# Kernel tuning notes

Measured on AMD Instinct MI355X. Metric: run time of the kernel, lower is better.

## Reference

```python
import jax, jax.numpy as jnp
import numpy as np

N = 100000      # nodes
E = 1000000     # edges
IN = 512
H = [512, 256]
C = 64          # n_classes
K = 10          # propagation steps
ALPHA = 0.1


def _glorot(key, shape):
    lim = np.sqrt(6.0 / (shape[0] + shape[1])).astype(np.float32)
    return jax.random.uniform(key, shape, jnp.float32, -lim, lim)


def setup_inputs() -> dict:
    key = jax.random.key(0)
    ks = jax.random.split(key, 6)
    features = jax.random.normal(ks[0], (N, IN), jnp.float32)
    edge_index = jax.random.randint(ks[1], (2, E), 0, N)  # int32/64 src,dst
    W0 = _glorot(ks[2], (H[0], IN)); b0 = jnp.zeros((H[0],), jnp.float32)
    W1 = _glorot(ks[3], (H[1], H[0])); b1 = jnp.zeros((H[1],), jnp.float32)
    W2 = _glorot(ks[4], (C, H[1])); b2 = jnp.zeros((C,), jnp.float32)
    return dict(features=features, edge_index=edge_index,
                W0=W0, b0=b0, W1=W1, b1=b1, W2=W2, b2=b2)


def _appnp(h, src, dst):
    # DGL APPNPConv: symmetric normalization D_out^{-1/2} A D_in^{-1/2},
    # degrees clamped to min 1; h_{t+1} = (1-a) * norm_agg + a * h_0.
    ones = jnp.ones(src.shape, h.dtype)
    deg_out = jax.ops.segment_sum(ones, src, num_segments=N)
    deg_in = jax.ops.segment_sum(ones, dst, num_segments=N)
    norm_src = jnp.maximum(deg_out, 1.0) ** -0.5  # [N]
    norm_dst = jnp.maximum(deg_in, 1.0) ** -0.5   # [N]
    h0 = h
    for _ in range(K):
        msg = (h * norm_src[:, None])[src]                     # [E, C] gather
        agg = jax.ops.segment_sum(msg, dst, num_segments=N)    # [N, C] scatter-add
        h = (1.0 - ALPHA) * agg * norm_dst[:, None] + ALPHA * h0
    return h


def reference(features, edge_index, W0, b0, W1, b1, W2, b2):
    src, dst = edge_index[0], edge_index[1]
    h = jax.nn.relu(features @ W0.T + b0)   # [N, 512]
    h = jax.nn.relu(h @ W1.T + b1)          # [N, 256]
    h = h @ W2.T + b2                       # [N, 64] logits
    return _appnp(h, src, dst)
```

## Files before the change

kernel.cpp:

```cpp
#include <hip/hip_runtime.h>
#include <hip/hip_bf16.h>

#define NN_NODES 100000
#define NE_EDGES 1000000
#define D_IN 512
#define D_H0 512
#define D_H1 256
#define D_C  64

using f32x4  = __attribute__((ext_vector_type(4))) float;
using h16x8  = __attribute__((ext_vector_type(8))) _Float16;

static __device__ __forceinline__ void gll16(const _Float16* g, _Float16* l){
    __builtin_amdgcn_global_load_lds(
        (const __attribute__((address_space(1))) unsigned int*)g,
        (__attribute__((address_space(3))) unsigned int*)l, 16, 0, 0);
}

__global__ __launch_bounds__(256) void tof16_tiled_kernel(
    const float* __restrict__ w, _Float16* __restrict__ o, int R, int K)
{
    int i = blockIdx.x * 256 + threadIdx.x;
    int n8 = R * (K >> 3);
    if (i >= n8) return;
    int kd = K >> 3;
    int r  = i / kd;
    int c0 = (i - r * kd) * 8;
    const f32x4 a = *(const f32x4*)(w + (size_t)r * K + c0);
    const f32x4 b = *(const f32x4*)(w + (size_t)r * K + c0 + 4);
    h16x8 h;
    #pragma unroll
    for (int j = 0; j < 4; j++){
        h[j]   = (_Float16)a[j];
        h[j+4] = (_Float16)b[j];
    }
    size_t off = ((size_t)(r >> 7) * (K >> 5) + (c0 >> 5)) * 4096
               + (size_t)(r & 127) * 32 + (c0 & 31);
    *(h16x8*)(o + off) = h;
}

template<bool RELU, int OMODE, int BN_T, int NBN, int KK>
__global__ __launch_bounds__(256, 4) void gemm_kernel(
    const _Float16* __restrict__ A,
    const _Float16* __restrict__ B,
    const float* __restrict__ bias,
    void* __restrict__ O1, _Float16* __restrict__ O2, const float* __restrict__ scale,
    int M, int NNc, int xq, int xr)
{
    constexpr int NTK  = KK / 32;
    constexpr int NF   = BN_T / 32;
    constexpr int BBLK = BN_T / 16;
    constexpr int TOT  = 8 + BBLK;
    constexpr int LPW  = TOT / 4;

    __shared__ _Float16 sA[2][128 * 32];
    __shared__ _Float16 sB[2][BN_T * 32];

    const int tid  = threadIdx.x;
    const int lane = tid & 63;
    const int wv   = tid >> 6;
    const int wm   = wv >> 1;
    const int wn   = wv & 1;
    const int fr   = lane & 15;
    const int fc   = lane >> 4;

    const int bid = blockIdx.x;
    const int xcd = bid & 7;
    const int i8  = bid >> 3;
    const int L   = ((xcd < xr) ? xcd * (xq + 1) : xr * (xq + 1) + (xcd - xr) * xq) + i8;
    const int mt  = L / NBN;
    const int bn  = L - mt * NBN;
    const int bm0 = mt * 128;
    const int bn0 = bn * BN_T;

    const int bslab = bn0 >> 7;
    const int binsl = bn0 & 127;

    const int loff = (lane >> 2) * 32 + ((lane & 3) ^ ((lane >> 3) & 3)) * 8;

    f32x4 acc[4][NF] = {};

    auto stage = [&](int b, int t){
        const _Float16* as = A + ((size_t)mt * NTK + t) * 4096;
        const _Float16* bs = B + ((size_t)bslab * NTK + t) * 4096 + binsl * 32;
        #pragma unroll
        for (int u = 0; u < LPW; u++){
            int idx = u * 4 + wv;
            if (idx < 8) gll16(as + idx * 512 + loff, sA[b] + idx * 512);
            else         gll16(bs + (idx - 8) * 512 + loff, sB[b] + (idx - 8) * 512);
        }
    };

    auto compute = [&](int b){
        h16x8 bf[NF];
        #pragma unroll
        for (int nf = 0; nf < NF; nf++){
            int r = wn * (BN_T / 2) + nf * 16 + fr;
            int c = (fc ^ ((r >> 1) & 3)) * 8;
            bf[nf] = *(const h16x8*)&sB[b][r * 32 + c];
        }
        h16x8 af[4];
        #pragma unroll
        for (int mf = 0; mf < 4; mf++){
            int r = wm * 64 + mf * 16 + fr;
            int c = (fc ^ ((r >> 1) & 3)) * 8;
            af[mf] = *(const h16x8*)&sA[b][r * 32 + c];
        }
        __builtin_amdgcn_s_setprio(1);
        #pragma unroll
        for (int mf = 0; mf < 4; mf++)
            #pragma unroll
            for (int nf = 0; nf < NF; nf++)
                acc[mf][nf] = __builtin_amdgcn_mfma_f32_16x16x32_f16(af[mf], bf[nf], acc[mf][nf], 0, 0, 0);
        __builtin_amdgcn_s_setprio(0);
    };

    stage(0, 0);
    __syncthreads();
    int cur = 0;
    for (int t = 0; t < NTK; t++){
        if (t + 1 < NTK) stage(cur ^ 1, t + 1);
        compute(cur);
        __syncthreads();
        cur ^= 1;
    }

    #pragma unroll
    for (int mf = 0; mf < 4; mf++){
        #pragma unroll
        for (int nf = 0; nf < NF; nf++){
            #pragma unroll
            for (int r = 0; r < 4; r++){
                int rg = bm0 + wm * 64 + mf * 16 + fc * 4 + r;
                int cg = bn0 + wn * (BN_T / 2) + nf * 16 + fr;
                if (rg < M){
                    float v = acc[mf][nf][r] + bias[cg];
                    if constexpr (RELU) v = fmaxf(v, 0.f);
                    if constexpr (OMODE == 1){
                        size_t o = ((size_t)mt * (NNc >> 5) + (cg >> 5)) * 4096
                                 + (size_t)(rg & 127) * 32 + (cg & 31);
                        ((_Float16*)O1)[o] = (_Float16)v;
                    } else {
                        ((_Float16*)O1)[(size_t)rg * NNc + cg] = (_Float16)v;
                        O2[(size_t)rg * NNc + cg] = (_Float16)(v * scale[rg]);
                    }
                }
            }
        }
    }
}

__global__ __launch_bounds__(512, 2) void gemm23_kernel(
    const _Float16* __restrict__ A,
    const _Float16* __restrict__ B1,
    const _Float16* __restrict__ B2,
    const float* __restrict__ bias1,
    const float* __restrict__ bias2,
    _Float16* __restrict__ h0h, _Float16* __restrict__ h0s,
    const float* __restrict__ nsrc,
    int M, int xq, int xr)
{
    constexpr int NTK = 16;
    __shared__ _Float16 smem[49152];

    const int tid  = threadIdx.x;
    const int lane = tid & 63;
    const int wv   = tid >> 6;
    const int wm   = wv >> 2;
    const int wn   = wv & 3;
    const int fr   = lane & 15;
    const int fc   = lane >> 4;

    const int bid = blockIdx.x;
    const int xcd = bid & 7;
    const int i8  = bid >> 3;
    const int mt  = ((xcd < xr) ? xcd * (xq + 1) : xr * (xq + 1) + (xcd - xr) * xq) + i8;
    const int bm0 = mt * 128;

    const int loff = (lane >> 2) * 32 + ((lane & 3) ^ ((lane >> 3) & 3)) * 8;

    _Float16* sW2 = smem + 32768;

    #pragma unroll
    for (int u = 0; u < 4; u++){
        int idx = u * 8 + wv;
        int k = idx >> 2, rb = idx & 3;
        gll16(B2 + (size_t)k * 4096 + rb * 512 + loff, sW2 + k * 2048 + rb * 512);
    }

    auto sA = [&](int b){ return smem + b * 12288; };
    auto sB = [&](int b){ return smem + b * 12288 + 4096; };

    auto stage = [&](int b, int t){
        #pragma unroll
        for (int u = 0; u < 3; u++){
            int idx = u * 8 + wv;
            if (idx < 8){
                gll16(A + ((size_t)mt * NTK + t) * 4096 + idx * 512 + loff,
                      sA(b) + idx * 512);
            } else {
                int rb = idx - 8;
                gll16(B1 + ((size_t)(rb >> 3) * NTK + t) * 4096 + (rb & 7) * 512 + loff,
                      sB(b) + rb * 512);
            }
        }
    };

    f32x4 acc[4][4] = {};

    auto compute = [&](int b){
        h16x8 bf[4];
        #pragma unroll
        for (int nf = 0; nf < 4; nf++){
            int r = wn * 64 + nf * 16 + fr;
            int c = (fc ^ ((r >> 1) & 3)) * 8;
            bf[nf] = *(const h16x8*)&sB(b)[r * 32 + c];
        }
        h16x8 af[4];
        #pragma unroll
        for (int mf = 0; mf < 4; mf++){
            int r = wm * 64 + mf * 16 + fr;
            int c = (fc ^ ((r >> 1) & 3)) * 8;
            af[mf] = *(const h16x8*)&sA(b)[r * 32 + c];
        }
        __builtin_amdgcn_s_setprio(1);
        #pragma unroll
        for (int mf = 0; mf < 4; mf++)
            #pragma unroll
            for (int nf = 0; nf < 4; nf++)
                acc[mf][nf] = __builtin_amdgcn_mfma_f32_16x16x32_f16(af[mf], bf[nf], acc[mf][nf], 0, 0, 0);
        __builtin_amdgcn_s_setprio(0);
    };

    stage(0, 0);
    __syncthreads();
    int cur = 0;
    for (int t = 0; t < NTK; t++){
        if (t + 1 < NTK) stage(cur ^ 1, t + 1);
        compute(cur);
        __syncthreads();
        cur ^= 1;
    }

    #pragma unroll
    for (int mf = 0; mf < 4; mf++){
        #pragma unroll
        for (int nf = 0; nf < 4; nf++){
            #pragma unroll
            for (int r = 0; r < 4; r++){
                int row = wm * 64 + mf * 16 + fc * 4 + r;
                int col = wn * 64 + nf * 16 + fr;
                float v = fmaxf(acc[mf][nf][r] + bias1[col], 0.f);
                int ci = col & 31;
                int sw = ((ci >> 3) ^ ((row >> 1) & 3)) * 8 + (ci & 7);
                smem[(col >> 5) * 4096 + row * 32 + sw] = (_Float16)v;
            }
        }
    }
    __syncthreads();

    f32x4 acc2[4] = {};
    #pragma unroll
    for (int kk = 0; kk < 8; kk++){
        int ar = wv * 16 + fr;
        int ac = (fc ^ ((ar >> 1) & 3)) * 8;
        h16x8 af = *(const h16x8*)&smem[kk * 4096 + ar * 32 + ac];
        #pragma unroll
        for (int nf = 0; nf < 4; nf++){
            int br = nf * 16 + fr;
            int bc = (fc ^ ((br >> 1) & 3)) * 8;
            h16x8 bf = *(const h16x8*)&sW2[kk * 2048 + br * 32 + bc];
            acc2[nf] = __builtin_amdgcn_mfma_f32_16x16x32_f16(af, bf, acc2[nf], 0, 0, 0);
        }
    }
    #pragma unroll
    for (int nf = 0; nf < 4; nf++){
        #pragma unroll
        for (int r = 0; r < 4; r++){
            int rg = bm0 + wv * 16 + fc * 4 + r;
            int cg = nf * 16 + fr;
            if (rg < M){
                float v = acc2[nf][r] + bias2[cg];
                h0h[(size_t)rg * D_C + cg] = (_Float16)v;
                h0s[(size_t)rg * D_C + cg] = (_Float16)(v * nsrc[rg]);
            }
        }
    }
}

__global__ void degrees_kernel(const int* __restrict__ src, const int* __restrict__ dst,
                               int* __restrict__ dout, int* __restrict__ din){
    int e = blockIdx.x * blockDim.x + threadIdx.x;
    if (e < NE_EDGES){
        atomicAdd(&dout[src[e]], 1);
        atomicAdd(&din[dst[e]], 1);
    }
}

__global__ void norm_kernel(const int* __restrict__ dout, const int* __restrict__ din,
                            float* __restrict__ ns, float* __restrict__ nd, int n){
    int i = blockIdx.x * blockDim.x + threadIdx.x;
    if (i < n){
        ns[i] = rsqrtf((float)(dout[i] > 1 ? dout[i] : 1));
        nd[i] = rsqrtf((float)(din[i]  > 1 ? din[i]  : 1));
    }
}

__global__ __launch_bounds__(256) void scan1_kernel(const int* __restrict__ din,
                                                    int* __restrict__ part,
                                                    int* __restrict__ bsum, int n){
    __shared__ int s[256];
    int i = blockIdx.x * 256 + threadIdx.x;
    int v = (i < n) ? din[i] : 0;
    s[threadIdx.x] = v;
    __syncthreads();
    for (int off = 1; off < 256; off <<= 1){
        int t = (threadIdx.x >= off) ? s[threadIdx.x - off] : 0;
        __syncthreads();
        s[threadIdx.x] += t;
        __syncthreads();
    }
    if (i < n) part[i] = s[threadIdx.x];
    if (threadIdx.x == 255) bsum[blockIdx.x] = s[255];
}

__global__ __launch_bounds__(512) void scan2_kernel(int* __restrict__ bsum, int nb){
    __shared__ int s[512];
    int v = (threadIdx.x < nb) ? bsum[threadIdx.x] : 0;
    s[threadIdx.x] = v;
    __syncthreads();
    for (int off = 1; off < 512; off <<= 1){
        int t = (threadIdx.x >= off) ? s[threadIdx.x - off] : 0;
        __syncthreads();
        s[threadIdx.x] += t;
        __syncthreads();
    }
    if (threadIdx.x < nb) bsum[threadIdx.x] = s[threadIdx.x];
}

__global__ void scan3_kernel(const int* __restrict__ part, const int* __restrict__ din,
                             const int* __restrict__ bsum, int* __restrict__ offs,
                             int* __restrict__ cur, int n){
    int i = blockIdx.x * 256 + threadIdx.x;
    if (i < n){
        int base = (blockIdx.x > 0) ? bsum[blockIdx.x - 1] : 0;
        int excl = base + part[i] - din[i];
        offs[i] = excl;
        cur[i]  = excl;
    }
}

__global__ void fill_kernel(const int* __restrict__ src, const int* __restrict__ dst,
                            int* __restrict__ cur, int* __restrict__ csr){
    int e = blockIdx.x * blockDim.x + threadIdx.x;
    if (e < NE_EDGES){
        int d = dst[e];
        int pos = atomicAdd(&cur[d], 1);
        csr[pos] = src[e];
    }
}

__global__ __launch_bounds__(256) void propagate_kernel(
    const _Float16* __restrict__ hs, const _Float16* __restrict__ h0h,
    float* __restrict__ hout, _Float16* __restrict__ houts,
    const int* __restrict__ offs, const int* __restrict__ din,
    const int* __restrict__ csr,
    const float* __restrict__ ns, const float* __restrict__ nd)
{
    int t    = blockIdx.x * 256 + threadIdx.x;
    int node = t >> 3;
    int gl   = t & 7;
    if (node >= NN_NODES) return;
    int start = offs[node];
    int deg   = din[node];
    float ndv = 0.9f * nd[node];
    float nsv = ns[node];
    h16x8 h0v = *(const h16x8*)(h0h + (size_t)node * D_C + gl * 8);
    float acc[8] = {};
    int j = 0;
    for (; j + 4 <= deg; j += 4){
        int s0 = csr[start + j];
        int s1 = csr[start + j + 1];
        int s2 = csr[start + j + 2];
        int s3 = csr[start + j + 3];
        h16x8 v0 = *(const h16x8*)(hs + (size_t)s0 * D_C + gl * 8);
        h16x8 v1 = *(const h16x8*)(hs + (size_t)s1 * D_C + gl * 8);
        h16x8 v2 = *(const h16x8*)(hs + (size_t)s2 * D_C + gl * 8);
        h16x8 v3 = *(const h16x8*)(hs + (size_t)s3 * D_C + gl * 8);
        #pragma unroll
        for (int i = 0; i < 8; i++)
            acc[i] += ((float)v0[i] + (float)v1[i]) + ((float)v2[i] + (float)v3[i]);
    }
    for (; j < deg; j++){
        int s0 = csr[start + j];
        h16x8 v0 = *(const h16x8*)(hs + (size_t)s0 * D_C + gl * 8);
        #pragma unroll
        for (int i = 0; i < 8; i++) acc[i] += (float)v0[i];
    }
    float out[8];
    #pragma unroll
    for (int i = 0; i < 8; i++) out[i] = acc[i] * ndv + 0.1f * (float)h0v[i];
    if (houts){
        h16x8 o;
        #pragma unroll
        for (int i = 0; i < 8; i++) o[i] = (_Float16)(out[i] * nsv);
        *(h16x8*)(houts + (size_t)node * D_C + gl * 8) = o;
    }
    if (hout){
        f32x4 oa, ob;
        #pragma unroll
        for (int i = 0; i < 4; i++){ oa[i] = out[i]; ob[i] = out[i + 4]; }
        *(f32x4*)(hout + (size_t)node * D_C + gl * 8)     = oa;
        *(f32x4*)(hout + (size_t)node * D_C + gl * 8 + 4) = ob;
    }
}

extern "C" void kernel_launch(void* const* d_in, const int* in_sizes, int n_in,
                              void* d_out, int out_size, void* d_ws, size_t ws_size,
                              hipStream_t stream)
{
    const float* features = (const float*)d_in[0];
    const int*   edge     = (const int*)d_in[1];
    const float* W0 = (const float*)d_in[2];
    const float* b0 = (const float*)d_in[3];
    const float* W1 = (const float*)d_in[4];
    const float* b1 = (const float*)d_in[5];
    const float* W2 = (const float*)d_in[6];
    const float* b2 = (const float*)d_in[7];
    const int* src = edge;
    const int* dst = edge + NE_EDGES;

    char* p = (char*)d_ws;
    auto alloc = [&](size_t bytes) -> char* {
        char* r = p;
        p += (bytes + 255) & ~(size_t)255;
        return r;
    };

    const int MT = (NN_NODES + 127) / 128;
    const size_t FEAT_T = (size_t)MT * 16 * 4096 * 2;
    const size_t HBUFH  = (size_t)NN_NODES * D_C * 2;

    _Float16* w0f = (_Float16*)alloc((size_t)4 * 16 * 4096 * 2);
    _Float16* w1f = (_Float16*)alloc((size_t)2 * 16 * 4096 * 2);
    _Float16* w2f = (_Float16*)alloc((size_t)1 * 8  * 4096 * 2);
    char* R1 = alloc(FEAT_T);
    char* R2 = alloc(FEAT_T);
    int*   deg_out = (int*)alloc((size_t)NN_NODES * 4);
    int*   deg_in  = (int*)alloc((size_t)NN_NODES * 4);
    float* nsrc    = (float*)alloc((size_t)NN_NODES * 4);
    float* ndst    = (float*)alloc((size_t)NN_NODES * 4);
    int*   part    = (int*)alloc((size_t)NN_NODES * 4);
    int*   bsum    = (int*)alloc(2048);
    int*   offs    = (int*)alloc((size_t)NN_NODES * 4);
    int*   cur     = (int*)alloc((size_t)NN_NODES * 4);
    int*   csr     = (int*)alloc((size_t)NE_EDGES * 4);
    if ((size_t)(p - (char*)d_ws) > ws_size) return;

    _Float16* fhf  = (_Float16*)R1;
    _Float16* act1 = (_Float16*)R2;
    _Float16* h0h  = (_Float16*)R1;
    _Float16* h0s  = (_Float16*)(R1 + HBUFH);
    _Float16* hAs  = (_Float16*)(R1 + 2 * HBUFH);
    _Float16* hBs  = (_Float16*)(R1 + 3 * HBUFH);

    hipMemsetAsync(deg_out, 0, (size_t)NN_NODES * 4, stream);
    hipMemsetAsync(deg_in,  0, (size_t)NN_NODES * 4, stream);
    degrees_kernel<<<(NE_EDGES + 255) / 256, 256, 0, stream>>>(src, dst, deg_out, deg_in);
    norm_kernel<<<(NN_NODES + 255) / 256, 256, 0, stream>>>(deg_out, deg_in, nsrc, ndst, NN_NODES);
    int nb = (NN_NODES + 255) / 256;
    scan1_kernel<<<nb, 256, 0, stream>>>(deg_in, part, bsum, NN_NODES);
    scan2_kernel<<<1, 512, 0, stream>>>(bsum, nb);
    scan3_kernel<<<nb, 256, 0, stream>>>(part, deg_in, bsum, offs, cur, NN_NODES);
    fill_kernel<<<(NE_EDGES + 255) / 256, 256, 0, stream>>>(src, dst, cur, csr);

    tof16_tiled_kernel<<<(NN_NODES * D_IN / 8 + 255) / 256, 256, 0, stream>>>(
        features, fhf, NN_NODES, D_IN);
    tof16_tiled_kernel<<<(D_H0 * D_IN / 8 + 255) / 256, 256, 0, stream>>>(W0, w0f, D_H0, D_IN);
    tof16_tiled_kernel<<<(D_H1 * D_H0 / 8 + 255) / 256, 256, 0, stream>>>(W1, w1f, D_H1, D_H0);
    tof16_tiled_kernel<<<(D_C * D_H1 / 8 + 255) / 256, 256, 0, stream>>>(W2, w2f, D_C, D_H1);

    {
        int nwg = MT * 8;
        gemm_kernel<true, 1, 64, 8, 512><<<nwg, 256, 0, stream>>>(
            fhf, w0f, b0, act1, nullptr, nullptr, NN_NODES, D_H0, nwg / 8, nwg % 8);
    }
    {
        int nwg = MT;
        gemm23_kernel<<<nwg, 512, 0, stream>>>(
            act1, w1f, w2f, b1, b2, h0h, h0s, nsrc, NN_NODES, nwg / 8, nwg % 8);
    }

    const _Float16* curs = h0s;
    _Float16* bufss[2] = { hAs, hBs };
    int pb = (NN_NODES * 8 + 255) / 256;
    for (int it = 0; it < 10; it++){
        float*    out  = (it == 9) ? (float*)d_out : nullptr;
        _Float16* outs = (it == 9) ? nullptr       : bufss[it & 1];
        propagate_kernel<<<pb, 256, 0, stream>>>(curs, h0h, out, outs, offs, deg_in, csr, nsrc, ndst);
        curs = outs;
    }
}
```

Baseline: 620.2 us.

## Fuse fp32-to-fp16 feature conversion into first GEMM's tile loading

Removes the standalone kernel that converted the 100000x512 feature matrix to tiled fp16. The first GEMM now stages fp32 feature rows into LDS with a swizzled layout and converts them to fp16 when forming MFMA operands. This avoids writing and re-reading an intermediate fp16 copy, at the cost of doubled A-tile LDS usage (possibly lower occupancy), extra conversion instructions per tile, and larger fp32 reads repeated across column blocks.

```diff
diff --git a/kernel.cpp b/kernel.cpp
--- a/kernel.cpp
+++ b/kernel.cpp
@@ -12,6 +12,11 @@
 using h16x8  = __attribute__((ext_vector_type(8))) _Float16;
 
 static __device__ __forceinline__ void gll16(const _Float16* g, _Float16* l){
+    __builtin_amdgcn_global_load_lds(
+        (const __attribute__((address_space(1))) unsigned int*)g,
+        (__attribute__((address_space(3))) unsigned int*)l, 16, 0, 0);
+}
+static __device__ __forceinline__ void gll16f(const float* g, float* l){
     __builtin_amdgcn_global_load_lds(
         (const __attribute__((address_space(1))) unsigned int*)g,
         (__attribute__((address_space(3))) unsigned int*)l, 16, 0, 0);
@@ -39,21 +44,16 @@
     *(h16x8*)(o + off) = h;
 }
 
-template<bool RELU, int OMODE, int BN_T, int NBN, int KK>
-__global__ __launch_bounds__(256, 4) void gemm_kernel(
-    const _Float16* __restrict__ A,
+__global__ __launch_bounds__(256, 4) void gemm1_kernel(
+    const float* __restrict__ A,
     const _Float16* __restrict__ B,
     const float* __restrict__ bias,
-    void* __restrict__ O1, _Float16* __restrict__ O2, const float* __restrict__ scale,
+    _Float16* __restrict__ O1,
     int M, int NNc, int xq, int xr)
 {
-    constexpr int NTK  = KK / 32;
-    constexpr int NF   = BN_T / 32;
-    constexpr int BBLK = BN_T / 16;
-    constexpr int TOT  = 8 + BBLK;
-    constexpr int LPW  = TOT / 4;
-
-    __shared__ _Float16 sA[2][128 * 32];
+    constexpr int KK = 512, NTK = 16, BN_T = 64, NBN = 8, NF = 2;
+
+    __shared__ float    sA[2][128 * 32];
     __shared__ _Float16 sB[2][BN_T * 32];
 
     const int tid  = threadIdx.x;
@@ -76,18 +76,26 @@
     const int bslab = bn0 >> 7;
     const int binsl = bn0 & 127;
 
-    const int loff = (lane >> 2) * 32 + ((lane & 3) ^ ((lane >> 3) & 3)) * 8;
+    const int lrowA = lane >> 3;
+    const int cfA   = ((((lane & 7) >> 1) ^ ((lane >> 3) & 3)) << 3) + (lane & 1) * 4;
+    const int loffB = (lane >> 2) * 32 + ((lane & 3) ^ ((lane >> 3) & 3)) * 8;
 
     f32x4 acc[4][NF] = {};
 
     auto stage = [&](int b, int t){
-        const _Float16* as = A + ((size_t)mt * NTK + t) * 4096;
+        const int k0 = t * 32;
         const _Float16* bs = B + ((size_t)bslab * NTK + t) * 4096 + binsl * 32;
         #pragma unroll
-        for (int u = 0; u < LPW; u++){
+        for (int u = 0; u < 5; u++){
             int idx = u * 4 + wv;
-            if (idx < 8) gll16(as + idx * 512 + loff, sA[b] + idx * 512);
-            else         gll16(bs + (idx - 8) * 512 + loff, sB[b] + (idx - 8) * 512);
+            if (idx < 16){
+                int g = bm0 + idx * 8 + lrowA;
+                if (g > M - 1) g = M - 1;
+                gll16f(A + (size_t)g * KK + k0 + cfA, sA[b] + idx * 256);
+            } else {
+                int rb = idx - 16;
+                gll16(bs + rb * 512 + loffB, sB[b] + rb * 512);
+            }
         }
     };
 
@@ -103,8 +111,15 @@
         #pragma unroll
         for (int mf = 0; mf < 4; mf++){
             int r = wm * 64 + mf * 16 + fr;
-            int c = (fc ^ ((r >> 1) & 3)) * 8;
-            af[mf] = *(const h16x8*)&sA[b][r * 32 + c];
+            int u = fc ^ (r & 3);
+            const float* pa = &sA[b][r * 32 + u * 8];
+            f32x4 lo = *(const f32x4*)pa;
+            f32x4 hi = *(const f32x4*)(pa + 4);
+            #pragma unroll
+            for (int j = 0; j < 4; j++){
+                af[mf][j]     = (_Float16)lo[j];
+                af[mf][j + 4] = (_Float16)hi[j];
+            }
         }
         __builtin_amdgcn_s_setprio(1);
         #pragma unroll
@@ -134,16 +149,10 @@
                 int rg = bm0 + wm * 64 + mf * 16 + fc * 4 + r;
                 int cg = bn0 + wn * (BN_T / 2) + nf * 16 + fr;
                 if (rg < M){
-                    float v = acc[mf][nf][r] + bias[cg];
-                    if constexpr (RELU) v = fmaxf(v, 0.f);
-                    if constexpr (OMODE == 1){
-                        size_t o = ((size_t)mt * (NNc >> 5) + (cg >> 5)) * 4096
-                                 + (size_t)(rg & 127) * 32 + (cg & 31);
-                        ((_Float16*)O1)[o] = (_Float16)v;
-                    } else {
-                        ((_Float16*)O1)[(size_t)rg * NNc + cg] = (_Float16)v;
-                        O2[(size_t)rg * NNc + cg] = (_Float16)(v * scale[rg]);
-                    }
+                    float v = fmaxf(acc[mf][nf][r] + bias[cg], 0.f);
+                    size_t o = ((size_t)mt * (NNc >> 5) + (cg >> 5)) * 4096
+                             + (size_t)(rg & 127) * 32 + (cg & 31);
+                    O1[o] = (_Float16)v;
                 }
             }
         }
@@ -457,7 +466,6 @@
     int*   csr     = (int*)alloc((size_t)NE_EDGES * 4);
     if ((size_t)(p - (char*)d_ws) > ws_size) return;
 
-    _Float16* fhf  = (_Float16*)R1;
     _Float16* act1 = (_Float16*)R2;
     _Float16* h0h  = (_Float16*)R1;
     _Float16* h0s  = (_Float16*)(R1 + HBUFH);
@@ -474,16 +482,14 @@
     scan3_kernel<<<nb, 256, 0, stream>>>(part, deg_in, bsum, offs, cur, NN_NODES);
     fill_kernel<<<(NE_EDGES + 255) / 256, 256, 0, stream>>>(src, dst, cur, csr);
 
-    tof16_tiled_kernel<<<(NN_NODES * D_IN / 8 + 255) / 256, 256, 0, stream>>>(
-        features, fhf, NN_NODES, D_IN);
     tof16_tiled_kernel<<<(D_H0 * D_IN / 8 + 255) / 256, 256, 0, stream>>>(W0, w0f, D_H0, D_IN);
     tof16_tiled_kernel<<<(D_H1 * D_H0 / 8 + 255) / 256, 256, 0, stream>>>(W1, w1f, D_H1, D_H0);
     tof16_tiled_kernel<<<(D_C * D_H1 / 8 + 255) / 256, 256, 0, stream>>>(W2, w2f, D_C, D_H1);
 
     {
         int nwg = MT * 8;
-        gemm_kernel<true, 1, 64, 8, 512><<<nwg, 256, 0, stream>>>(
-            fhf, w0f, b0, act1, nullptr, nullptr, NN_NODES, D_H0, nwg / 8, nwg % 8);
+        gemm1_kernel<<<nwg, 256, 0, stream>>>(
+            features, w0f, b0, act1, NN_NODES, D_H0, nwg / 8, nwg % 8);
     }
     {
         int nwg = MT;
```

After: 652.8 us. 5.2% more time.
